# Optimization experiments

Hardware: AMD Instinct MI355X
Metric: run time of the kernel (lower is better)

Reference implementation:

```python
import jax, jax.numpy as jnp
import numpy as np

B, S, D = 4, 2048, 1024
H = 16
HD = D // H  # head_dim = 64
EPS = 1e-6   # flax LayerNorm default epsilon


def _layernorm(x, scale, bias):
    # per-head LayerNorm over last axis (head_dim), computed in fp32
    x32 = x.astype(jnp.float32)
    mu = jnp.mean(x32, axis=-1, keepdims=True)
    var = jnp.mean(jnp.square(x32 - mu), axis=-1, keepdims=True)
    y = (x32 - mu) * jax.lax.rsqrt(var + EPS)
    return (y * scale + bias).astype(x.dtype)


def setup_inputs() -> dict:
    key = jax.random.key(0)
    ks = jax.random.split(key, 8)
    std = 1.0 / np.sqrt(D)
    return {
        "inputs_q": jax.random.normal(ks[0], (B, S, D), jnp.float32),
        "inputs_kv": jax.random.normal(ks[1], (B, S, D), jnp.float32),
        "Wq": jax.random.normal(ks[2], (D, D), jnp.float32) * std,
        "bq": jnp.zeros((D,), jnp.float32),
        "Wk": jax.random.normal(ks[3], (D, D), jnp.float32) * std,
        "bk": jnp.zeros((D,), jnp.float32),
        "Wv": jax.random.normal(ks[4], (D, D), jnp.float32) * std,
        "bv": jnp.zeros((D,), jnp.float32),
        "q_scale": jnp.ones((HD,), jnp.float32),
        "q_bias": jnp.zeros((HD,), jnp.float32),
        "k_scale": jnp.ones((HD,), jnp.float32),
        "k_bias": jnp.zeros((HD,), jnp.float32),
        "v_scale": jnp.ones((HD,), jnp.float32),
        "v_bias": jnp.zeros((HD,), jnp.float32),
        "Wo": jax.random.normal(ks[5], (D, D), jnp.float32) * std,
        "bo": jnp.zeros((D,), jnp.float32),
    }


def reference(inputs_q, inputs_kv, Wq, bq, Wk, bk, Wv, bv,
              q_scale, q_bias, k_scale, k_bias, v_scale, v_bias, Wo, bo):
    b, s, _ = inputs_q.shape
    # QKV projections, reshape to (b, s, h, hd)
    q = (inputs_q @ Wq + bq).reshape(b, s, H, HD)
    k = (inputs_kv @ Wk + bk).reshape(b, s, H, HD)
    v = (inputs_kv @ Wv + bv).reshape(b, s, H, HD)
    # per-head LayerNorm in fp32
    q = _layernorm(q, q_scale, q_bias)
    k = _layernorm(k, k_scale, k_bias)
    v = _layernorm(v, v_scale, v_bias)
    # attention: scores (b, h, s, s)
    scores = jnp.einsum('bqhd,bkhd->bhqk', q, k) / jnp.sqrt(jnp.asarray(HD, q.dtype))
    attn = jax.nn.softmax(scores, axis=-1)
    out = jnp.einsum('bhqk,bkhd->bqhd', attn, v).reshape(b, s, D)
    return out @ Wo + bo
```

## Files before the change

### kernel.cpp

```cpp
#include <hip/hip_runtime.h>
#include <hip/hip_bf16.h>
#include <stdint.h>

#define B_   4
#define S_   2048
#define D_   1024
#define H_   16
#define HD_  64
#define M_   8192
#define LN_EPS 1e-6f

typedef __attribute__((ext_vector_type(4))) float  f32x4;
typedef __attribute__((ext_vector_type(8))) __bf16 bf16x8;

__device__ __forceinline__ unsigned short f2bf(float f) {
  unsigned int u = __float_as_uint(f);
  u += 0x7FFFu + ((u >> 16) & 1u);
  return (unsigned short)(u >> 16);
}

typedef const unsigned int __attribute__((address_space(1)))* gas1_t;
typedef unsigned int __attribute__((address_space(3)))*       las3_t;

__device__ __forceinline__ void gload_lds16(const void* g, void* l) {
  __builtin_amdgcn_global_load_lds((gas1_t)(uintptr_t)g,
                                   (las3_t)(unsigned int)(uintptr_t)l, 16, 0, 0);
}

__global__ void castk(const float* __restrict__ src, unsigned short* __restrict__ dst, int n4) {
  int stride = gridDim.x * blockDim.x;
  for (int i = blockIdx.x * blockDim.x + threadIdx.x; i < n4; i += stride) {
    float4 v = ((const float4*)src)[i];
    ushort4 o;
    o.x = f2bf(v.x); o.y = f2bf(v.y); o.z = f2bf(v.z); o.w = f2bf(v.w);
    ((ushort4*)dst)[i] = o;
  }
}

__global__ void wcast(const float* __restrict__ W, unsigned short* __restrict__ Wt) {
  __shared__ float tile[32][33];
  int tx = threadIdx.x & 31, ty = threadIdx.x >> 5;
  int n0 = blockIdx.x * 32, k0 = blockIdx.y * 32;
  #pragma unroll
  for (int r = ty; r < 32; r += 8)
    tile[r][tx] = W[(size_t)(k0 + r) * D_ + n0 + tx];
  __syncthreads();
  #pragma unroll
  for (int r = ty; r < 32; r += 8)
    Wt[(size_t)(n0 + r) * D_ + k0 + tx] = f2bf(tile[tx][r]);
}

template <int LN>
__global__ __launch_bounds__(256, 2) void gemm_bt(
    const unsigned short* __restrict__ A,
    const unsigned short* __restrict__ Bt,
    const float* __restrict__ bias,
    const float* __restrict__ lnsc,
    const float* __restrict__ lnbi,
    void* __restrict__ Cout)
{
  __shared__ __align__(16) unsigned short lA[128 * 32];
  __shared__ __align__(16) unsigned short lB[128 * 32];
  const int tid  = threadIdx.x;
  const int wid  = tid >> 6, lane = tid & 63;
  const int lg   = lane >> 4, li = lane & 15;
  const int m0   = blockIdx.x * 128, n0 = blockIdx.y * 128;
  const int wr   = wid >> 1, wc = wid & 1;

  f32x4 acc[4][4] = {};

  const int srow = wid * 32 + (lane >> 2);
  const int sc8  = (lane & 3) * 8;

  for (int kt = 0; kt < 32; ++kt) {
    const int k0 = kt * 32;
    #pragma unroll
    for (int i = 0; i < 2; ++i) {
      gload_lds16(A  + (size_t)(m0 + srow + i * 16) * 1024 + k0 + sc8, &lA[(wid * 2 + i) * 512]);
      gload_lds16(Bt + (size_t)(n0 + srow + i * 16) * 1024 + k0 + sc8, &lB[(wid * 2 + i) * 512]);
    }
    __syncthreads();
    bf16x8 af[4], bfr[4];
    #pragma unroll
    for (int mi = 0; mi < 4; ++mi)
      af[mi] = *(const bf16x8*)&lA[(wr * 64 + mi * 16 + li) * 32 + lg * 8];
    #pragma unroll
    for (int nj = 0; nj < 4; ++nj)
      bfr[nj] = *(const bf16x8*)&lB[(wc * 64 + nj * 16 + li) * 32 + lg * 8];
    #pragma unroll
    for (int mi = 0; mi < 4; ++mi)
      #pragma unroll
      for (int nj = 0; nj < 4; ++nj)
        acc[mi][nj] = __builtin_amdgcn_mfma_f32_16x16x32_bf16(af[mi], bfr[nj], acc[mi][nj], 0, 0, 0);
    __syncthreads();
  }

  const int rowb = m0 + wr * 64;
  const int nb   = n0 + wc * 64;
  if (LN) {
    float bia[4], scl[4], lnb[4];
    #pragma unroll
    for (int nj = 0; nj < 4; ++nj) {
      int col = nb + nj * 16 + li;
      bia[nj] = bias[col];
      scl[nj] = lnsc[col & 63];
      lnb[nj] = lnbi[col & 63];
    }
    unsigned short* C = (unsigned short*)Cout;
    #pragma unroll
    for (int mi = 0; mi < 4; ++mi) {
      #pragma unroll
      for (int r = 0; r < 4; ++r) {
        float x[4]; float s1 = 0.f, s2 = 0.f;
        #pragma unroll
        for (int nj = 0; nj < 4; ++nj) {
          x[nj] = acc[mi][nj][r] + bia[nj];
          s1 += x[nj]; s2 += x[nj] * x[nj];
        }
        #pragma unroll
        for (int msk = 1; msk < 16; msk <<= 1) {
          s1 += __shfl_xor(s1, msk);
          s2 += __shfl_xor(s2, msk);
        }
        float mu  = s1 * (1.f / 64.f);
        float var = fmaxf(s2 * (1.f / 64.f) - mu * mu, 0.f);
        float inv = rsqrtf(var + LN_EPS);
        size_t row = (size_t)(rowb + mi * 16 + lg * 4 + r);
        #pragma unroll
        for (int nj = 0; nj < 4; ++nj) {
          float y = (x[nj] - mu) * inv * scl[nj] + lnb[nj];
          C[row * 1024 + nb + nj * 16 + li] = f2bf(y);
        }
      }
    }
  } else {
    float bia[4];
    #pragma unroll
    for (int nj = 0; nj < 4; ++nj) bia[nj] = bias[nb + nj * 16 + li];
    float* C = (float*)Cout;
    #pragma unroll
    for (int mi = 0; mi < 4; ++mi)
      #pragma unroll
      for (int r = 0; r < 4; ++r) {
        size_t row = (size_t)(rowb + mi * 16 + lg * 4 + r);
        #pragma unroll
        for (int nj = 0; nj < 4; ++nj)
          C[row * 1024 + nb + nj * 16 + li] = acc[mi][nj][r] + bia[nj];
      }
  }
}

__global__ __launch_bounds__(256) void vtrans(const unsigned short* __restrict__ V,
                                              unsigned short* __restrict__ VT) {
  __shared__ __align__(16) unsigned short t[64][72];
  int bh = blockIdx.y, b = bh >> 4, h = bh & 15;
  int s0 = blockIdx.x * 64;
  int tid = threadIdx.x;
  #pragma unroll
  for (int it = 0; it < 2; ++it) {
    int cid = it * 256 + tid;
    int r = cid >> 3, c = (cid & 7) * 8;
    int4 v = *(const int4*)(V + (size_t)(b * 2048 + s0 + r) * 1024 + h * 64 + c);
    *(int4*)(&t[r][c]) = v;
  }
  __syncthreads();
  #pragma unroll
  for (int it = 0; it < 2; ++it) {
    int cid = it * 256 + tid;
    int hd = cid >> 3, sc = (cid & 7) * 8;
    alignas(16) unsigned short tmp[8];
    #pragma unroll
    for (int j = 0; j < 8; ++j) tmp[j] = t[sc + j][hd];
    *(int4*)(VT + ((size_t)bh * 64 + hd) * 2048 + s0 + sc) = *(int4*)tmp;
  }
}

__global__ __launch_bounds__(256, 2) void attn(
    const unsigned short* __restrict__ Q, const unsigned short* __restrict__ K,
    const unsigned short* __restrict__ VT, unsigned short* __restrict__ AO)
{
  __shared__ __align__(16) unsigned short Ks[128 * 64];
  __shared__ __align__(16) unsigned short Vs[64 * 128];
  __shared__ __align__(16) unsigned short Ps[4][32 * 128];
  const int tid = threadIdx.x, wid = tid >> 6, lane = tid & 63;
  const int lg = lane >> 4, li = lane & 15;
  const int qt = blockIdx.x, bh = blockIdx.y, b = bh >> 4, h = bh & 15;

  bf16x8 qf[2][2];
  const int qrow0 = b * 2048 + qt * 128 + wid * 32;
  #pragma unroll
  for (int mi = 0; mi < 2; ++mi)
    #pragma unroll
    for (int kc = 0; kc < 2; ++kc)
      qf[mi][kc] = *(const bf16x8*)(Q + (size_t)(qrow0 + mi * 16 + li) * 1024 + h * 64 + kc * 32 + lg * 8);

  f32x4 o[2][4] = {};
  float mrun[2][4], lrun[2][4];
  #pragma unroll
  for (int mi = 0; mi < 2; ++mi)
    #pragma unroll
    for (int r = 0; r < 4; ++r) { mrun[mi][r] = -1e30f; lrun[mi][r] = 0.f; }

  unsigned short* Pw = &Ps[wid][0];

  for (int kt = 0; kt < 16; ++kt) {
    #pragma unroll
    for (int i = 0; i < 4; ++i) {
      int cid = (wid * 4 + i) * 64 + lane;
      int r = cid >> 3, c = cid & 7;
      gload_lds16(K + (size_t)(b * 2048 + kt * 128 + r) * 1024 + h * 64 + ((c ^ (r & 7)) << 3),
                  &Ks[(wid * 4 + i) * 512]);
    }
    #pragma unroll
    for (int i = 0; i < 4; ++i) {
      int cid = (wid * 4 + i) * 64 + lane;
      int r = cid >> 4, c = cid & 15;
      gload_lds16(VT + ((size_t)bh * 64 + r) * 2048 + kt * 128 + ((c ^ (r & 7)) << 3),
                  &Vs[(wid * 4 + i) * 512]);
    }
    __syncthreads();

    f32x4 sacc[2][8] = {};
    #pragma unroll
    for (int kc = 0; kc < 2; ++kc)
      #pragma unroll
      for (int nj = 0; nj < 8; ++nj) {
        int key = nj * 16 + li;
        int slot = (kc * 4 + lg) ^ (key & 7);
        bf16x8 kb = *(const bf16x8*)&Ks[key * 64 + slot * 8];
        #pragma unroll
        for (int mi = 0; mi < 2; ++mi)
          sacc[mi][nj] = __builtin_amdgcn_mfma_f32_16x16x32_bf16(qf[mi][kc], kb, sacc[mi][nj], 0, 0, 0);
      }

    #pragma unroll
    for (int mi = 0; mi < 2; ++mi) {
      #pragma unroll
      for (int r = 0; r < 4; ++r) {
        float tm = -1e30f;
        #pragma unroll
        for (int nj = 0; nj < 8; ++nj) tm = fmaxf(tm, sacc[mi][nj][r]);
        tm *= 0.125f;
        #pragma unroll
        for (int msk = 1; msk < 16; msk <<= 1) tm = fmaxf(tm, __shfl_xor(tm, msk));
        float mnew  = fmaxf(mrun[mi][r], tm);
        float alpha = __expf(mrun[mi][r] - mnew);
        mrun[mi][r] = mnew;
        lrun[mi][r] *= alpha;
        #pragma unroll
        for (int nj = 0; nj < 4; ++nj) o[mi][nj][r] *= alpha;
        float ls = 0.f;
        int row = mi * 16 + lg * 4 + r;
        #pragma unroll
        for (int nj = 0; nj < 8; ++nj) {
          float p = __expf(sacc[mi][nj][r] * 0.125f - mnew);
          ls += p;
          int col  = nj * 16 + li;
          int slot = (col >> 3) ^ (row & 7);
          Pw[row * 128 + slot * 8 + (col & 7)] = f2bf(p);
        }
        #pragma unroll
        for (int msk = 1; msk < 16; msk <<= 1) ls += __shfl_xor(ls, msk);
        lrun[mi][r] += ls;
      }
    }
    __syncthreads();

    #pragma unroll
    for (int kc = 0; kc < 4; ++kc) {
      bf16x8 pa[2];
      #pragma unroll
      for (int mi = 0; mi < 2; ++mi) {
        int row = mi * 16 + li;
        int slot = (kc * 4 + lg) ^ (row & 7);
        pa[mi] = *(const bf16x8*)&Pw[row * 128 + slot * 8];
      }
      #pragma unroll
      for (int nj = 0; nj < 4; ++nj) {
        int d = nj * 16 + li;
        int slot = (kc * 4 + lg) ^ (d & 7);
        bf16x8 vb = *(const bf16x8*)&Vs[d * 128 + slot * 8];
        #pragma unroll
        for (int mi = 0; mi < 2; ++mi)
          o[mi][nj] = __builtin_amdgcn_mfma_f32_16x16x32_bf16(pa[mi], vb, o[mi][nj], 0, 0, 0);
      }
    }
    __syncthreads();
  }

  #pragma unroll
  for (int mi = 0; mi < 2; ++mi)
    #pragma unroll
    for (int r = 0; r < 4; ++r) {
      float inv = 1.0f / lrun[mi][r];
      size_t rowg = (size_t)(qrow0 + mi * 16 + lg * 4 + r);
      #pragma unroll
      for (int nj = 0; nj < 4; ++nj)
        AO[rowg * 1024 + h * 64 + nj * 16 + li] = f2bf(o[mi][nj][r] * inv);
    }
}

extern "C" void kernel_launch(void* const* d_in, const int* in_sizes, int n_in,
                              void* d_out, int out_size, void* d_ws, size_t ws_size,
                              hipStream_t stream) {
  const float* inq  = (const float*)d_in[0];
  const float* inkv = (const float*)d_in[1];
  const float* Wq   = (const float*)d_in[2];
  const float* bq   = (const float*)d_in[3];
  const float* Wk   = (const float*)d_in[4];
  const float* bk   = (const float*)d_in[5];
  const float* Wv   = (const float*)d_in[6];
  const float* bv   = (const float*)d_in[7];
  const float* qs   = (const float*)d_in[8];
  const float* qb   = (const float*)d_in[9];
  const float* ksc  = (const float*)d_in[10];
  const float* kbi  = (const float*)d_in[11];
  const float* vsc  = (const float*)d_in[12];
  const float* vbi  = (const float*)d_in[13];
  const float* Wo   = (const float*)d_in[14];
  const float* bo   = (const float*)d_in[15];
  float* out = (float*)d_out;

  char* ws = (char*)d_ws;
  const size_t MB = 1024 * 1024;
  unsigned short* Xq  = (unsigned short*)(ws + 0);
  unsigned short* Xkv = (unsigned short*)(ws + 16 * MB);
  unsigned short* Wqt = (unsigned short*)(ws + 32 * MB);
  unsigned short* Wkt = (unsigned short*)(ws + 34 * MB);
  unsigned short* Wvt = (unsigned short*)(ws + 36 * MB);
  unsigned short* Wot = (unsigned short*)(ws + 38 * MB);
  unsigned short* Qb  = (unsigned short*)(ws + 40 * MB);
  unsigned short* Kb  = (unsigned short*)(ws + 56 * MB);
  unsigned short* Vb  = (unsigned short*)(ws + 72 * MB);
  unsigned short* VT  = Xkv;
  unsigned short* AO  = Xq;

  castk<<<2048, 256, 0, stream>>>(inq,  Xq,  M_ * D_ / 4);
  castk<<<2048, 256, 0, stream>>>(inkv, Xkv, M_ * D_ / 4);
  wcast<<<dim3(32, 32), 256, 0, stream>>>(Wq, Wqt);
  wcast<<<dim3(32, 32), 256, 0, stream>>>(Wk, Wkt);
  wcast<<<dim3(32, 32), 256, 0, stream>>>(Wv, Wvt);
  wcast<<<dim3(32, 32), 256, 0, stream>>>(Wo, Wot);

  gemm_bt<1><<<dim3(64, 8), 256, 0, stream>>>(Xq,  Wqt, bq, qs,  qb,  (void*)Qb);
  gemm_bt<1><<<dim3(64, 8), 256, 0, stream>>>(Xkv, Wkt, bk, ksc, kbi, (void*)Kb);
  gemm_bt<1><<<dim3(64, 8), 256, 0, stream>>>(Xkv, Wvt, bv, vsc, vbi, (void*)Vb);

  vtrans<<<dim3(32, 64), 256, 0, stream>>>(Vb, VT);
  attn<<<dim3(16, 64), 256, 0, stream>>>(Qb, Kb, VT, AO);

  gemm_bt<0><<<dim3(64, 8), 256, 0, stream>>>(AO, Wot, bo, nullptr, nullptr, (void*)out);
}
```

Baseline: 455.3 us.

## Rewrite attention with 32x32 MFMA, register-resident P, and exp2-folded scaling

The attention kernel switches to 32x32x16 MFMA, computing S^T so that P stays in registers, exchanged across lane halves with a shuffle instead of going through an LDS staging buffer. The softmax scale and log2(e) are folded into the Q projection epilogue, so the kernel can use raw v_exp_f32. Rescaling of the running output is skipped unless the block max rises by more than 8. The kernel also adds a block-index swizzle, setprio hints around the MFMA groups, and a higher occupancy target. The lazy rescale depends on the bf16 and fp32 ranges tolerating probabilities up to 2^8 before the final normalisation, and the higher launch bound may cause register spills.

```diff
diff --git a/kernel.cpp b/kernel.cpp
--- a/kernel.cpp
+++ b/kernel.cpp
@@ -10,13 +10,26 @@
 #define M_   8192
 #define LN_EPS 1e-6f
 
-typedef __attribute__((ext_vector_type(4))) float  f32x4;
-typedef __attribute__((ext_vector_type(8))) __bf16 bf16x8;
+typedef __attribute__((ext_vector_type(4)))  float  f32x4;
+typedef __attribute__((ext_vector_type(16))) float  f32x16;
+typedef __attribute__((ext_vector_type(8)))  __bf16 bf16x8;
 
 __device__ __forceinline__ unsigned short f2bf(float f) {
   unsigned int u = __float_as_uint(f);
   u += 0x7FFFu + ((u >> 16) & 1u);
   return (unsigned short)(u >> 16);
+}
+
+__device__ __forceinline__ unsigned int cvtpk(float a, float b) {
+  unsigned int r;
+  asm("v_cvt_pk_bf16_f32 %0, %1, %2" : "=v"(r) : "v"(a), "v"(b));
+  return r;
+}
+
+__device__ __forceinline__ float exp2a(float x) {
+  float r;
+  asm("v_exp_f32 %0, %1" : "=v"(r) : "v"(x));
+  return r;
 }
 
 typedef const unsigned int __attribute__((address_space(1)))* gas1_t;
@@ -57,6 +70,7 @@
     const float* __restrict__ bias,
     const float* __restrict__ lnsc,
     const float* __restrict__ lnbi,
+    float oscale,
     void* __restrict__ Cout)
 {
   __shared__ __align__(16) unsigned short lA[128 * 32];
@@ -103,8 +117,8 @@
     for (int nj = 0; nj < 4; ++nj) {
       int col = nb + nj * 16 + li;
       bia[nj] = bias[col];
-      scl[nj] = lnsc[col & 63];
-      lnb[nj] = lnbi[col & 63];
+      scl[nj] = lnsc[col & 63] * oscale;
+      lnb[nj] = lnbi[col & 63] * oscale;
     }
     unsigned short* C = (unsigned short*)Cout;
     #pragma unroll
@@ -175,33 +189,28 @@
   }
 }
 
-__global__ __launch_bounds__(256, 2) void attn(
+__global__ __launch_bounds__(256, 4) void attn(
     const unsigned short* __restrict__ Q, const unsigned short* __restrict__ K,
     const unsigned short* __restrict__ VT, unsigned short* __restrict__ AO)
 {
   __shared__ __align__(16) unsigned short Ks[128 * 64];
   __shared__ __align__(16) unsigned short Vs[64 * 128];
-  __shared__ __align__(16) unsigned short Ps[4][32 * 128];
   const int tid = threadIdx.x, wid = tid >> 6, lane = tid & 63;
-  const int lg = lane >> 4, li = lane & 15;
-  const int qt = blockIdx.x, bh = blockIdx.y, b = bh >> 4, h = bh & 15;
-
-  bf16x8 qf[2][2];
+  const int hi = lane >> 5, lq = lane & 31;
+
+  const int bid = blockIdx.x;
+  const int swz = (bid & 7) * 128 + (bid >> 3);
+  const int qt = swz & 15, bh = swz >> 4, b = bh >> 4, h = bh & 15;
+
   const int qrow0 = b * 2048 + qt * 128 + wid * 32;
-  #pragma unroll
-  for (int mi = 0; mi < 2; ++mi)
-    #pragma unroll
-    for (int kc = 0; kc < 2; ++kc)
-      qf[mi][kc] = *(const bf16x8*)(Q + (size_t)(qrow0 + mi * 16 + li) * 1024 + h * 64 + kc * 32 + lg * 8);
-
-  f32x4 o[2][4] = {};
-  float mrun[2][4], lrun[2][4];
-  #pragma unroll
-  for (int mi = 0; mi < 2; ++mi)
-    #pragma unroll
-    for (int r = 0; r < 4; ++r) { mrun[mi][r] = -1e30f; lrun[mi][r] = 0.f; }
-
-  unsigned short* Pw = &Ps[wid][0];
+
+  bf16x8 qf[4];
+  #pragma unroll
+  for (int c = 0; c < 4; ++c)
+    qf[c] = *(const bf16x8*)(Q + (size_t)(qrow0 + lq) * 1024 + h * 64 + c * 16 + hi * 8);
+
+  f32x16 oacc[2] = {};
+  float m = -3.0e38f, l = 0.f;
 
   for (int kt = 0; kt < 16; ++kt) {
     #pragma unroll
@@ -220,83 +229,81 @@
     }
     __syncthreads();
 
-    f32x4 sacc[2][8] = {};
-    #pragma unroll
-    for (int kc = 0; kc < 2; ++kc)
-      #pragma unroll
-      for (int nj = 0; nj < 8; ++nj) {
-        int key = nj * 16 + li;
-        int slot = (kc * 4 + lg) ^ (key & 7);
-        bf16x8 kb = *(const bf16x8*)&Ks[key * 64 + slot * 8];
-        #pragma unroll
-        for (int mi = 0; mi < 2; ++mi)
-          sacc[mi][nj] = __builtin_amdgcn_mfma_f32_16x16x32_bf16(qf[mi][kc], kb, sacc[mi][nj], 0, 0, 0);
-      }
-
-    #pragma unroll
-    for (int mi = 0; mi < 2; ++mi) {
-      #pragma unroll
-      for (int r = 0; r < 4; ++r) {
-        float tm = -1e30f;
-        #pragma unroll
-        for (int nj = 0; nj < 8; ++nj) tm = fmaxf(tm, sacc[mi][nj][r]);
-        tm *= 0.125f;
-        #pragma unroll
-        for (int msk = 1; msk < 16; msk <<= 1) tm = fmaxf(tm, __shfl_xor(tm, msk));
-        float mnew  = fmaxf(mrun[mi][r], tm);
-        float alpha = __expf(mrun[mi][r] - mnew);
-        mrun[mi][r] = mnew;
-        lrun[mi][r] *= alpha;
-        #pragma unroll
-        for (int nj = 0; nj < 4; ++nj) o[mi][nj][r] *= alpha;
-        float ls = 0.f;
-        int row = mi * 16 + lg * 4 + r;
-        #pragma unroll
-        for (int nj = 0; nj < 8; ++nj) {
-          float p = __expf(sacc[mi][nj][r] * 0.125f - mnew);
-          ls += p;
-          int col  = nj * 16 + li;
-          int slot = (col >> 3) ^ (row & 7);
-          Pw[row * 128 + slot * 8 + (col & 7)] = f2bf(p);
+    #pragma unroll
+    for (int kb = 0; kb < 4; ++kb) {
+      f32x16 sacc = {};
+      __builtin_amdgcn_s_setprio(1);
+      #pragma unroll
+      for (int c = 0; c < 4; ++c) {
+        int key = kb * 32 + lq;
+        int slot = (c * 2 + hi) ^ (key & 7);
+        bf16x8 kf = *(const bf16x8*)&Ks[key * 64 + slot * 8];
+        sacc = __builtin_amdgcn_mfma_f32_32x32x16_bf16(kf, qf[c], sacc, 0, 0, 0);
+      }
+      __builtin_amdgcn_s_setprio(0);
+
+      float bmax = sacc[0];
+      #pragma unroll
+      for (int r = 1; r < 16; ++r) bmax = fmaxf(bmax, sacc[r]);
+      bmax = fmaxf(bmax, __shfl_xor(bmax, 32));
+
+      if (bmax > m + 8.f) {
+        float alpha = exp2a(m - bmax);
+        m = bmax;
+        l *= alpha;
+        #pragma unroll
+        for (int db = 0; db < 2; ++db)
+          #pragma unroll
+          for (int r = 0; r < 16; ++r) oacc[db][r] *= alpha;
+      }
+
+      float ls = 0.f;
+      #pragma unroll
+      for (int r = 0; r < 16; ++r) {
+        float e = exp2a(sacc[r] - m);
+        sacc[r] = e; ls += e;
+      }
+      l += ls;
+
+      unsigned int W[8], X[8];
+      #pragma unroll
+      for (int i = 0; i < 8; ++i) W[i] = cvtpk(sacc[2 * i], sacc[2 * i + 1]);
+      #pragma unroll
+      for (int i = 0; i < 8; ++i) X[i] = (unsigned int)__shfl_xor((int)W[i], 32);
+
+      #pragma unroll
+      for (int c2 = 0; c2 < 2; ++c2) {
+        const int i0 = c2 * 4;
+        union { unsigned int u[4]; bf16x8 v; } pf;
+        pf.u[0] = hi ? X[i0 + 2] : W[i0];
+        pf.u[1] = hi ? X[i0 + 3] : W[i0 + 1];
+        pf.u[2] = hi ? W[i0 + 2] : X[i0];
+        pf.u[3] = hi ? W[i0 + 3] : X[i0 + 1];
+        __builtin_amdgcn_s_setprio(1);
+        #pragma unroll
+        for (int db = 0; db < 2; ++db) {
+          int d = db * 32 + lq;
+          int chunk = kb * 4 + c2 * 2 + hi;
+          int slot = chunk ^ (d & 7);
+          bf16x8 vf = *(const bf16x8*)&Vs[d * 128 + slot * 8];
+          oacc[db] = __builtin_amdgcn_mfma_f32_32x32x16_bf16(vf, pf.v, oacc[db], 0, 0, 0);
         }
-        #pragma unroll
-        for (int msk = 1; msk < 16; msk <<= 1) ls += __shfl_xor(ls, msk);
-        lrun[mi][r] += ls;
+        __builtin_amdgcn_s_setprio(0);
       }
     }
     __syncthreads();
-
-    #pragma unroll
-    for (int kc = 0; kc < 4; ++kc) {
-      bf16x8 pa[2];
-      #pragma unroll
-      for (int mi = 0; mi < 2; ++mi) {
-        int row = mi * 16 + li;
-        int slot = (kc * 4 + lg) ^ (row & 7);
-        pa[mi] = *(const bf16x8*)&Pw[row * 128 + slot * 8];
-      }
-      #pragma unroll
-      for (int nj = 0; nj < 4; ++nj) {
-        int d = nj * 16 + li;
-        int slot = (kc * 4 + lg) ^ (d & 7);
-        bf16x8 vb = *(const bf16x8*)&Vs[d * 128 + slot * 8];
-        #pragma unroll
-        for (int mi = 0; mi < 2; ++mi)
-          o[mi][nj] = __builtin_amdgcn_mfma_f32_16x16x32_bf16(pa[mi], vb, o[mi][nj], 0, 0, 0);
-      }
-    }
-    __syncthreads();
-  }
-
-  #pragma unroll
-  for (int mi = 0; mi < 2; ++mi)
-    #pragma unroll
-    for (int r = 0; r < 4; ++r) {
-      float inv = 1.0f / lrun[mi][r];
-      size_t rowg = (size_t)(qrow0 + mi * 16 + lg * 4 + r);
-      #pragma unroll
-      for (int nj = 0; nj < 4; ++nj)
-        AO[rowg * 1024 + h * 64 + nj * 16 + li] = f2bf(o[mi][nj][r] * inv);
+  }
+
+  l += __shfl_xor(l, 32);
+  float linv = 1.f / l;
+  #pragma unroll
+  for (int db = 0; db < 2; ++db)
+    #pragma unroll
+    for (int g = 0; g < 4; ++g) {
+      unsigned int w0 = cvtpk(oacc[db][4 * g] * linv,     oacc[db][4 * g + 1] * linv);
+      unsigned int w1 = cvtpk(oacc[db][4 * g + 2] * linv, oacc[db][4 * g + 3] * linv);
+      uint2 wv; wv.x = w0; wv.y = w1;
+      *(uint2*)(AO + (size_t)(qrow0 + lq) * 1024 + h * 64 + db * 32 + g * 8 + hi * 4) = wv;
     }
 }
 
@@ -335,6 +342,8 @@
   unsigned short* VT  = Xkv;
   unsigned short* AO  = Xq;
 
+  const float K2 = 0.18033688011112042f;
+
   castk<<<2048, 256, 0, stream>>>(inq,  Xq,  M_ * D_ / 4);
   castk<<<2048, 256, 0, stream>>>(inkv, Xkv, M_ * D_ / 4);
   wcast<<<dim3(32, 32), 256, 0, stream>>>(Wq, Wqt);
@@ -342,12 +351,12 @@
   wcast<<<dim3(32, 32), 256, 0, stream>>>(Wv, Wvt);
   wcast<<<dim3(32, 32), 256, 0, stream>>>(Wo, Wot);
 
-  gemm_bt<1><<<dim3(64, 8), 256, 0, stream>>>(Xq,  Wqt, bq, qs,  qb,  (void*)Qb);
-  gemm_bt<1><<<dim3(64, 8), 256, 0, stream>>>(Xkv, Wkt, bk, ksc, kbi, (void*)Kb);
-  gemm_bt<1><<<dim3(64, 8), 256, 0, stream>>>(Xkv, Wvt, bv, vsc, vbi, (void*)Vb);
+  gemm_bt<1><<<dim3(64, 8), 256, 0, stream>>>(Xq,  Wqt, bq, qs,  qb,  K2,  (void*)Qb);
+  gemm_bt<1><<<dim3(64, 8), 256, 0, stream>>>(Xkv, Wkt, bk, ksc, kbi, 1.0f, (void*)Kb);
+  gemm_bt<1><<<dim3(64, 8), 256, 0, stream>>>(Xkv, Wvt, bv, vsc, vbi, 1.0f, (void*)Vb);
 
   vtrans<<<dim3(32, 64), 256, 0, stream>>>(Vb, VT);
-  attn<<<dim3(16, 64), 256, 0, stream>>>(Qb, Kb, VT, AO);
-
-  gemm_bt<0><<<dim3(64, 8), 256, 0, stream>>>(AO, Wot, bo, nullptr, nullptr, (void*)out);
-}
+  attn<<<1024, 256, 0, stream>>>(Qb, Kb, VT, AO);
+
+  gemm_bt<0><<<dim3(64, 8), 256, 0, stream>>>(AO, Wot, bo, nullptr, nullptr, 1.0f, (void*)out);
+}
```

Measured after the change: 367.9 us. -19.2%, faster.
